# Kernel optimization log

Hardware: AMD Instinct MI355X
Metric: run time of the kernel (lower is better)

Reference implementation:

```python
import jax, jax.numpy as jnp
import numpy as np

LAST_Q = 64      # queries used for dynamic pattern estimation (MInference default)
V_TOPK = 1024    # number of vertical (column) indices kept
S_TOPK = 2048    # number of slash (diagonal) offsets kept
FORCE_V = 30     # first columns always kept
FORCE_S = 100    # most-recent diagonals always kept


def setup_inputs() -> dict:
    key = jax.random.key(0)
    kq, kk, kv = jax.random.split(key, 3)
    B, H, S, D = 1, 8, 4096, 128
    q = jax.random.normal(kq, (B, H, S, D), dtype=jnp.float32)
    k = jax.random.normal(kk, (B, H, S, D), dtype=jnp.float32)
    v = jax.random.normal(kv, (B, H, S, D), dtype=jnp.float32)
    return {"q": q, "k": k, "v": v}


def _vertical_slash_attention(q, k, v):
    B, H, S, D = q.shape
    scale = 1.0 / np.sqrt(D).astype(np.float32)

    # ---- pattern estimation on the last LAST_Q queries ----
    qk = jnp.einsum('bhqd,bhkd->bhqk', q[:, :, -LAST_Q:], k) * scale  # [B,H,LQ,S]
    qpos = S - LAST_Q + jnp.arange(LAST_Q)                            # query positions
    causal_last = qpos[:, None] >= jnp.arange(S)[None, :]             # [LQ,S]
    qk = jnp.where(causal_last, qk, jnp.finfo(qk.dtype).min)
    qk = jax.nn.softmax(qk, axis=-1)

    # vertical (column) scores
    vertical = qk.sum(axis=2)                                         # [B,H,S]
    vertical = vertical.at[..., :FORCE_V].set(jnp.inf)
    v_idx = jax.lax.top_k(vertical, V_TOPK)[1]                        # column ids [B,H,V_TOPK]

    # slash (diagonal) scores, indexed by distance o = i - j in [0, S)
    dist = qpos[:, None] - jnp.arange(S)[None, :]                     # [LQ,S]
    dist_c = jnp.clip(dist, 0, S - 1)
    slash = jnp.zeros((B, H, S), qk.dtype).at[:, :, dist_c].add(
        jnp.where(dist >= 0, qk, 0.0))                                # [B,H,S]
    slash = slash.at[..., :FORCE_S].set(jnp.inf)
    s_off = jax.lax.top_k(slash, S_TOPK)[1]                           # diagonal offsets [B,H,S_TOPK]

    # ---- build vertical-slash sparsity mask ----
    ar = jnp.arange(S)
    v_mask = (v_idx[..., :, None] == ar).any(axis=-2)                 # [B,H,S] column allowed
    s_mask = (s_off[..., :, None] == ar).any(axis=-2)                 # [B,H,S] offset allowed

    dmat = ar[:, None] - ar[None, :]                                  # [S,S] query-key distance
    causal = dmat >= 0
    allowed = causal & (v_mask[:, :, None, :] | s_mask[:, :, jnp.clip(dmat, 0, S - 1)])

    # ---- sparse (mask-equivalent) attention ----
    scores = jnp.einsum('bhqd,bhkd->bhqk', q, k) * scale              # [B,H,S,S]
    scores = jnp.where(allowed, scores, jnp.finfo(scores.dtype).min)
    probs = jax.nn.softmax(scores, axis=-1)
    return jnp.einsum('bhqk,bhkd->bhqd', probs, v)


def reference(q, k, v):
    return _vertical_slash_attention(q, k, v)
```

## Files before the change

kernel.cpp:

```cpp
#include <hip/hip_runtime.h>
#include <hip/hip_bf16.h>
#include <math.h>

#define S_LEN 4096
#define DHEAD 128
#define NHEAD 8
#define LASTQ 64
#define V_TOPK 1024
#define S_TOPK 2048
#define FORCE_V 30
#define FORCE_S 100

#define SCALE 0.08838834764831845f
#define NEGBIG -3.0e38f

typedef __attribute__((ext_vector_type(8))) short short8;
typedef __attribute__((ext_vector_type(4))) float floatx4;
typedef unsigned long long u64;

__device__ __forceinline__ unsigned short f2bf(float f) {
    unsigned u = __float_as_uint(f);
    unsigned r = (u + 0x7fffu + ((u >> 16) & 1u)) >> 16;
    return (unsigned short)r;
}

__global__ __launch_bounds__(256) void cvt_bf16(const float* __restrict__ src,
                                                unsigned short* __restrict__ dst, int n4) {
    int i = blockIdx.x * 256 + threadIdx.x;
    if (i < n4) {
        float4 v = ((const float4*)src)[i];
        ushort4 o;
        o.x = f2bf(v.x); o.y = f2bf(v.y); o.z = f2bf(v.z); o.w = f2bf(v.w);
        ((ushort4*)dst)[i] = o;
    }
}

__global__ __launch_bounds__(256) void transpose_v(const float* __restrict__ v,
                                                   unsigned short* __restrict__ vt) {
    int bx = blockIdx.x;
    int h  = bx >> 7;
    int rem = bx & 127;
    int d0 = (rem >> 6) * 64;
    int k0 = (rem & 63) * 64;
    __shared__ __align__(16) unsigned short T[64][72];
    int t = threadIdx.x;
#pragma unroll
    for (int it = 0; it < 4; ++it) {
        int idx = t + it * 256;
        int r = idx >> 4, c4 = idx & 15;
        float4 val = *(const float4*)(v + ((size_t)(h * S_LEN) + k0 + r) * DHEAD + d0 + c4 * 4);
        T[c4 * 4 + 0][r] = f2bf(val.x);
        T[c4 * 4 + 1][r] = f2bf(val.y);
        T[c4 * 4 + 2][r] = f2bf(val.z);
        T[c4 * 4 + 3][r] = f2bf(val.w);
    }
    __syncthreads();
#pragma unroll
    for (int it = 0; it < 2; ++it) {
        int idx = t + it * 256;
        int r = idx >> 3, c8 = idx & 7;
        *(uint4*)(vt + ((size_t)h * DHEAD + d0 + r) * S_LEN + k0 + c8 * 8) = *(uint4*)&T[r][c8 * 8];
    }
}

__global__ __launch_bounds__(256) void score_qk(const float* __restrict__ q,
                                                const float* __restrict__ k,
                                                float* __restrict__ scores) {
    int h  = blockIdx.x >> 6;
    int kt = blockIdx.x & 63;
    int t  = threadIdx.x;
    int jl = t >> 2, part = t & 3;
    int j  = kt * 64 + jl;

    __shared__ float4 Qs[64 * 32];
    const float4* qbase = (const float4*)(q + ((size_t)h * S_LEN + (S_LEN - LASTQ)) * DHEAD);
    for (int idx = t; idx < 64 * 32; idx += 256) Qs[idx] = qbase[idx];
    __syncthreads();

    float4 kr[8];
    const float4* kp = (const float4*)(k + ((size_t)h * S_LEN + j) * DHEAD) + part * 8;
#pragma unroll
    for (int c = 0; c < 8; ++c) kr[c] = kp[c];

    float* sp = scores + (size_t)h * LASTQ * S_LEN + j;
#pragma unroll 4
    for (int qi = 0; qi < LASTQ; ++qi) {
        const float4* qp4 = Qs + qi * 32 + part * 8;
        float dot = 0.f;
#pragma unroll
        for (int c = 0; c < 8; ++c) {
            float4 a = qp4[c], b = kr[c];
            dot += a.x * b.x + a.y * b.y + a.z * b.z + a.w * b.w;
        }
        dot += __shfl_xor(dot, 1, 64);
        dot += __shfl_xor(dot, 2, 64);
        if (part == 0) {
            int qpos = S_LEN - LASTQ + qi;
            sp[(size_t)qi * S_LEN] = (j <= qpos) ? dot * SCALE : NEGBIG;
        }
    }
}

__global__ __launch_bounds__(256) void row_stats(const float* __restrict__ scores,
                                                 float* __restrict__ m_out,
                                                 float* __restrict__ inv_out) {
    int row  = blockIdx.x * 4 + (threadIdx.x >> 6);
    int lane = threadIdx.x & 63;
    const float4* rp = (const float4*)(scores + (size_t)row * S_LEN);
    float mx = NEGBIG;
    for (int i = lane; i < S_LEN / 4; i += 64) {
        float4 s4 = rp[i];
        mx = fmaxf(mx, fmaxf(fmaxf(s4.x, s4.y), fmaxf(s4.z, s4.w)));
    }
#pragma unroll
    for (int d = 32; d >= 1; d >>= 1) mx = fmaxf(mx, __shfl_xor(mx, d, 64));
    float su = 0.f;
    for (int i = lane; i < S_LEN / 4; i += 64) {
        float4 s4 = rp[i];
        su += __expf(s4.x - mx) + __expf(s4.y - mx) + __expf(s4.z - mx) + __expf(s4.w - mx);
    }
#pragma unroll
    for (int d = 32; d >= 1; d >>= 1) su += __shfl_xor(su, d, 64);
    if (lane == 0) { m_out[row] = mx; inv_out[row] = 1.0f / su; }
}

__global__ __launch_bounds__(256) void vs_accum(const float* __restrict__ scores,
                                                const float* __restrict__ m_all,
                                                const float* __restrict__ inv_all,
                                                float* __restrict__ vertical,
                                                float* __restrict__ slash) {
    int h     = blockIdx.x >> 3;
    int chunk = blockIdx.x & 7;
    int t = threadIdx.x;
    __shared__ float sm[LASTQ], sv[LASTQ];
    if (t < LASTQ) { sm[t] = m_all[h * LASTQ + t]; sv[t] = inv_all[h * LASTQ + t]; }
    __syncthreads();

    const float* S0 = scores + (size_t)h * LASTQ * S_LEN;
#pragma unroll
    for (int rep = 0; rep < 2; ++rep) {
        int j = chunk * 512 + rep * 256 + t;
        float vacc = 0.f, sacc = 0.f;
        for (int r = 0; r < LASTQ; ++r) {
            vacc += __expf(S0[(size_t)r * S_LEN + j] - sm[r]) * sv[r];
            int idx = (S_LEN - LASTQ) + r - j;
            if (idx >= 0)
                sacc += __expf(S0[(size_t)r * S_LEN + idx] - sm[r]) * sv[r];
        }
        vertical[h * S_LEN + j] = vacc;
        slash[h * S_LEN + j]    = sacc;
    }
}

__global__ __launch_bounds__(256) void topk_mask(const float* __restrict__ vertical,
                                                 const float* __restrict__ slash,
                                                 unsigned* __restrict__ col_mask,
                                                 unsigned* __restrict__ diag_mask) {
    int h   = blockIdx.x >> 1;
    int sel = blockIdx.x & 1;
    const float* src = sel ? (slash + h * S_LEN) : (vertical + h * S_LEN);
    unsigned* dst    = sel ? (diag_mask + h * (S_LEN / 32)) : (col_mask + h * (S_LEN / 32));
    int kwant  = sel ? S_TOPK : V_TOPK;
    int forced = sel ? FORCE_S : FORCE_V;
    int t = threadIdx.x;

    __shared__ unsigned keys[S_LEN];
    __shared__ int hist[256];
    __shared__ int sh_digit, sh_want;

    for (int j = t; j < S_LEN; j += 256) {
        float f = (j < forced) ? __builtin_inff() : src[j];
        unsigned u = __float_as_uint(f);
        u = (u & 0x80000000u) ? ~u : (u | 0x80000000u);
        keys[j] = u;
    }
    __syncthreads();

    unsigned prefix = 0;
    int want = kwant;
    for (int shift = 24; shift >= 0; shift -= 8) {
        hist[t] = 0;
        __syncthreads();
        for (int j = t; j < S_LEN; j += 256) {
            unsigned key = keys[j];
            bool match = (shift == 24) || (((key ^ prefix) >> (shift + 8)) == 0);
            if (match) atomicAdd(&hist[(key >> shift) & 255u], 1);
        }
        __syncthreads();
        if (t == 0) {
            int cum = 0, d = 255;
            for (; d >= 0; --d) {
                cum += hist[d];
                if (cum >= want) break;
            }
            sh_digit = d;
            sh_want  = want - (cum - hist[d]);
        }
        __syncthreads();
        prefix |= ((unsigned)sh_digit) << shift;
        want = sh_want;
        __syncthreads();
    }
    for (int w = t; w < S_LEN / 32; w += 256) {
        unsigned bits = 0;
        for (int b = 0; b < 32; ++b)
            if (keys[w * 32 + b] >= prefix) bits |= (1u << b);
        dst[w] = bits;
    }
}

#define KS_STRIDE 136
#define VT_STRIDE 72
#define PS_STRIDE 72

__global__ __launch_bounds__(256, 2) void sparse_attn_mfma(
        const unsigned short* __restrict__ qbf,
        const unsigned short* __restrict__ kbf,
        const unsigned short* __restrict__ vtbf,
        const unsigned* __restrict__ col_mask,
        const unsigned* __restrict__ diag_mask,
        float* __restrict__ pO, float* __restrict__ pm, float* __restrict__ pl) {
    int b = blockIdx.x;
    int h = b & 7;
    int j = b >> 3;
    int qt, c0g, c1g, cidx;
    if (j < 64) {
        qt = 63 - (j >> 1);
        int half = j & 1;
        int mid = (qt + 2) >> 1;
        cidx = half;
        c0g = half ? mid : 0;
        c1g = half ? (qt + 1) : mid;
    } else {
        qt = 95 - j;
        cidx = 0;
        c0g = 0;
        c1g = qt + 1;
    }
    int i0 = qt * 64;
    int t    = threadIdx.x;
    int wave = t >> 6;
    int lane = t & 63;
    int ln16 = lane & 15;
    int quad = lane >> 4;

    __shared__ __align__(16) unsigned short Ks[64 * KS_STRIDE];
    __shared__ __align__(16) unsigned short Vt[128 * VT_STRIDE];
    __shared__ __align__(16) unsigned short Ps[4 * 16 * PS_STRIDE];
    __shared__ u64 allowed[64];
    __shared__ unsigned dmLDS[130];

    if (t < 130) dmLDS[t] = (t < 128) ? diag_mask[h * 128 + t] : 0u;

    int qrow = i0 + wave * 16 + ln16;
    const unsigned short* qp = qbf + ((size_t)h * S_LEN + qrow) * DHEAD;
    short8 qf[4];
#pragma unroll
    for (int ds = 0; ds < 4; ++ds)
        qf[ds] = *(const short8*)(qp + ds * 32 + quad * 8);

    floatx4 o4[8];
#pragma unroll
    for (int n = 0; n < 8; ++n) o4[n] = (floatx4){0.f, 0.f, 0.f, 0.f};
    float m_run[4] = {NEGBIG, NEGBIG, NEGBIG, NEGBIG};
    float l_run[4] = {0.f, 0.f, 0.f, 0.f};

    unsigned short* psw = Ps + wave * 16 * PS_STRIDE;

    for (int jt = c0g; jt < c1g; ++jt) {
        int j0 = jt * 64;
        __syncthreads();

#pragma unroll
        for (int it = 0; it < 4; ++it) {
            int idx = t + it * 256;
            int r = idx >> 4, c8 = idx & 15;
            *(uint4*)&Ks[r * KS_STRIDE + c8 * 8] =
                *(const uint4*)(kbf + ((size_t)(h * S_LEN) + j0 + r) * DHEAD + c8 * 8);
        }
#pragma unroll
        for (int it = 0; it < 4; ++it) {
            int idx = t + it * 256;
            int r = idx >> 3, c8 = idx & 7;
            *(uint4*)&Vt[r * VT_STRIDE + c8 * 8] =
                *(const uint4*)(vtbf + ((size_t)h * DHEAD + r) * S_LEN + j0 + c8 * 8);
        }
        if (t < 64) {
            int i = i0 + t;
            int off0 = i - j0;
            u64 causal = (off0 >= 63) ? ~0ull : ((1ull << (off0 + 1)) - 1ull);
            u64 cwv = ((u64)col_mask[h * 128 + (j0 >> 5) + 1] << 32) |
                      (u64)col_mask[h * 128 + (j0 >> 5)];
            int sb = off0 - 63;
            u64 V;
            if (sb >= 0) {
                int w = sb >> 5, sh = sb & 31;
                u64 lo = ((u64)dmLDS[w + 1] << 32) | (u64)dmLDS[w];
                u64 hi = (u64)dmLDS[w + 2];
                V = (lo >> sh) | (sh ? (hi << (64 - sh)) : 0ull);
            } else {
                u64 w0 = ((u64)dmLDS[1] << 32) | (u64)dmLDS[0];
                V = w0 << (-sb);
            }
            allowed[t] = (cwv | __brevll(V)) & causal;
        }
        __syncthreads();

        floatx4 s_acc[4];
#pragma unroll
        for (int c = 0; c < 4; ++c) {
            s_acc[c] = (floatx4){0.f, 0.f, 0.f, 0.f};
            const unsigned short* kbase = Ks + (c * 16 + ln16) * KS_STRIDE + quad * 8;
#pragma unroll
            for (int ds = 0; ds < 4; ++ds) {
                short8 kf = *(const short8*)(kbase + ds * 32);
                s_acc[c] = __builtin_amdgcn_mfma_f32_16x16x32_bf16(qf[ds], kf, s_acc[c], 0, 0, 0);
            }
        }

        u64 Arow[4];
#pragma unroll
        for (int r = 0; r < 4; ++r)
            Arow[r] = allowed[wave * 16 + quad * 4 + r];
        float sc[4][4];
#pragma unroll
        for (int c = 0; c < 4; ++c)
#pragma unroll
            for (int r = 0; r < 4; ++r) {
                bool ok = (Arow[r] >> (c * 16 + ln16)) & 1ull;
                sc[c][r] = ok ? s_acc[c][r] * SCALE : -__builtin_inff();
            }

        float mnew[4], alpha[4];
#pragma unroll
        for (int r = 0; r < 4; ++r) {
            float mx = fmaxf(fmaxf(sc[0][r], sc[1][r]), fmaxf(sc[2][r], sc[3][r]));
#pragma unroll
            for (int d = 8; d >= 1; d >>= 1) mx = fmaxf(mx, __shfl_xor(mx, d, 64));
            mnew[r] = fmaxf(m_run[r], mx);
            alpha[r] = __expf(m_run[r] - mnew[r]);
            m_run[r] = mnew[r];
        }
        float pv[4][4];
#pragma unroll
        for (int r = 0; r < 4; ++r) {
            float su = 0.f;
#pragma unroll
            for (int c = 0; c < 4; ++c) {
                float p = __expf(sc[c][r] - mnew[r]);
                pv[c][r] = p;
                su += p;
            }
#pragma unroll
            for (int d = 8; d >= 1; d >>= 1) su += __shfl_xor(su, d, 64);
            l_run[r] = l_run[r] * alpha[r] + su;
        }
#pragma unroll
        for (int n = 0; n < 8; ++n)
#pragma unroll
            for (int r = 0; r < 4; ++r) o4[n][r] *= alpha[r];

#pragma unroll
        for (int c = 0; c < 4; ++c)
#pragma unroll
            for (int r = 0; r < 4; ++r)
                psw[(quad * 4 + r) * PS_STRIDE + c * 16 + ln16] = f2bf(pv[c][r]);
        asm volatile("" ::: "memory");
        short8 pf0 = *(const short8*)&psw[ln16 * PS_STRIDE + quad * 8];
        short8 pf1 = *(const short8*)&psw[ln16 * PS_STRIDE + 32 + quad * 8];

#pragma unroll
        for (int n = 0; n < 8; ++n) {
            const unsigned short* vbase = Vt + (n * 16 + ln16) * VT_STRIDE + quad * 8;
            short8 vf0 = *(const short8*)(vbase);
            short8 vf1 = *(const short8*)(vbase + 32);
            o4[n] = __builtin_amdgcn_mfma_f32_16x16x32_bf16(pf0, vf0, o4[n], 0, 0, 0);
            o4[n] = __builtin_amdgcn_mfma_f32_16x16x32_bf16(pf1, vf1, o4[n], 0, 0, 0);
        }
    }

    int pi = (h * 64 + qt) * 2 + cidx;
    float* pOp = pO + (size_t)pi * (64 * DHEAD);
#pragma unroll
    for (int r = 0; r < 4; ++r) {
        int row = wave * 16 + quad * 4 + r;
        if (ln16 == 0) { pm[pi * 64 + row] = m_run[r]; pl[pi * 64 + row] = l_run[r]; }
#pragma unroll
        for (int n = 0; n < 8; ++n)
            pOp[row * DHEAD + n * 16 + ln16] = o4[n][r];
    }
}

__global__ __launch_bounds__(256) void merge_out(const float* __restrict__ pO,
                                                 const float* __restrict__ pm,
                                                 const float* __restrict__ pl,
                                                 float* __restrict__ out) {
    int b = blockIdx.x;
    int qt = b & 63;
    int t = threadIdx.x;
    int row = t >> 2, cg = t & 3;
    int pi0 = b * 2;
    bool two = (qt >= 32);

    float m0 = pm[pi0 * 64 + row], l0 = pl[pi0 * 64 + row];
    float w0 = 1.f, w1 = 0.f, denom = l0;
    if (two) {
        float m1 = pm[(pi0 + 1) * 64 + row], l1 = pl[(pi0 + 1) * 64 + row];
        float ms = fmaxf(m0, m1);
        w0 = __expf(m0 - ms);
        w1 = __expf(m1 - ms);
        denom = w0 * l0 + w1 * l1;
    }
    float invl = 1.0f / denom;

    const float4* O0 = (const float4*)(pO + (size_t)pi0 * (64 * DHEAD) + row * DHEAD + cg * 32);
    const float4* O1 = (const float4*)((const float*)O0 + 64 * DHEAD);
    float4* op = (float4*)(out + ((size_t)b * 64 + row) * DHEAD + cg * 32);
#pragma unroll
    for (int i = 0; i < 8; ++i) {
        float4 a = O0[i];
        float4 c;
        if (two) {
            float4 bb = O1[i];
            c.x = (w0 * a.x + w1 * bb.x) * invl;
            c.y = (w0 * a.y + w1 * bb.y) * invl;
            c.z = (w0 * a.z + w1 * bb.z) * invl;
            c.w = (w0 * a.w + w1 * bb.w) * invl;
        } else {
            c.x = a.x * invl; c.y = a.y * invl; c.z = a.z * invl; c.w = a.w * invl;
        }
        op[i] = c;
    }
}

extern "C" void kernel_launch(void* const* d_in, const int* in_sizes, int n_in,
                              void* d_out, int out_size, void* d_ws, size_t ws_size,
                              hipStream_t stream) {
    const float* q = (const float*)d_in[0];
    const float* k = (const float*)d_in[1];
    const float* v = (const float*)d_in[2];
    float* out = (float*)d_out;

    float* vertical = (float*)d_ws;
    float* slash    = vertical + NHEAD * S_LEN;
    unsigned* col_m  = (unsigned*)(slash + NHEAD * S_LEN);
    unsigned* diag_m = col_m + NHEAD * (S_LEN / 32);
    float* m_all   = (float*)(diag_m + NHEAD * (S_LEN / 32));
    float* inv_all = m_all + NHEAD * LASTQ;
    unsigned short* qbf  = (unsigned short*)(inv_all + NHEAD * LASTQ);
    unsigned short* kbf  = qbf + (size_t)NHEAD * S_LEN * DHEAD;
    unsigned short* vtbf = kbf + (size_t)NHEAD * S_LEN * DHEAD;
    float* big = (float*)(vtbf + (size_t)NHEAD * S_LEN * DHEAD);
    float* scores = big;
    float* pO = big;
    float* pm = big + (size_t)1024 * 64 * DHEAD;
    float* pl = pm + 1024 * 64;

    int n4 = NHEAD * S_LEN * DHEAD / 4;
    cvt_bf16<<<(n4 + 255) / 256, 256, 0, stream>>>(q, qbf, n4);
    cvt_bf16<<<(n4 + 255) / 256, 256, 0, stream>>>(k, kbf, n4);
    transpose_v<<<NHEAD * 2 * (S_LEN / 64), 256, 0, stream>>>(v, vtbf);

    score_qk<<<NHEAD * 64, 256, 0, stream>>>(q, k, scores);
    row_stats<<<NHEAD * LASTQ / 4, 256, 0, stream>>>(scores, m_all, inv_all);
    vs_accum<<<NHEAD * 8, 256, 0, stream>>>(scores, m_all, inv_all, vertical, slash);
    topk_mask<<<NHEAD * 2, 256, 0, stream>>>(vertical, slash, col_m, diag_m);

    sparse_attn_mfma<<<NHEAD * 96, 256, 0, stream>>>(qbf, kbf, vtbf, col_m, diag_m, pO, pm, pl);
    merge_out<<<NHEAD * 64, 256, 0, stream>>>(pO, pm, pl, out);
}
```

Baseline: 362.2 us.

## Restructure sparse attention into 128-row query tiles with balanced split-K job table

The attention kernel now handles 128 query rows per block, with two 16-row sub-tiles per wave that share each K/V tile load. A static job table splits the causal key range into roughly equal chunks so blocks get balanced work. The Q bf16 conversion and scale are folded into the attention kernel, and the K convert and V transpose are merged into one prep launch. The vertical/slash accumulation is fused into the top-k kernel using 1024 threads, and partial outputs are stored as bf16 to cut merge traffic. In exchange, register pressure rises, and rounding the partial outputs to bf16 adds some precision loss.

```diff
diff --git a/kernel.cpp b/kernel.cpp
--- a/kernel.cpp
+++ b/kernel.cpp
@@ -14,6 +14,8 @@
 #define SCALE 0.08838834764831845f
 #define NEGBIG -3.0e38f
 
+#define NJOBS 111
+
 typedef __attribute__((ext_vector_type(8))) short short8;
 typedef __attribute__((ext_vector_type(4))) float floatx4;
 typedef unsigned long long u64;
@@ -23,43 +25,77 @@
     unsigned r = (u + 0x7fffu + ((u >> 16) & 1u)) >> 16;
     return (unsigned short)r;
 }
-
-__global__ __launch_bounds__(256) void cvt_bf16(const float* __restrict__ src,
-                                                unsigned short* __restrict__ dst, int n4) {
-    int i = blockIdx.x * 256 + threadIdx.x;
-    if (i < n4) {
-        float4 v = ((const float4*)src)[i];
-        ushort4 o;
-        o.x = f2bf(v.x); o.y = f2bf(v.y); o.z = f2bf(v.z); o.w = f2bf(v.w);
-        ((ushort4*)dst)[i] = o;
-    }
-}
-
-__global__ __launch_bounds__(256) void transpose_v(const float* __restrict__ v,
-                                                   unsigned short* __restrict__ vt) {
-    int bx = blockIdx.x;
-    int h  = bx >> 7;
-    int rem = bx & 127;
-    int d0 = (rem >> 6) * 64;
-    int k0 = (rem & 63) * 64;
-    __shared__ __align__(16) unsigned short T[64][72];
-    int t = threadIdx.x;
-#pragma unroll
-    for (int it = 0; it < 4; ++it) {
-        int idx = t + it * 256;
-        int r = idx >> 4, c4 = idx & 15;
-        float4 val = *(const float4*)(v + ((size_t)(h * S_LEN) + k0 + r) * DHEAD + d0 + c4 * 4);
-        T[c4 * 4 + 0][r] = f2bf(val.x);
-        T[c4 * 4 + 1][r] = f2bf(val.y);
-        T[c4 * 4 + 2][r] = f2bf(val.z);
-        T[c4 * 4 + 3][r] = f2bf(val.w);
-    }
-    __syncthreads();
-#pragma unroll
-    for (int it = 0; it < 2; ++it) {
-        int idx = t + it * 256;
-        int r = idx >> 3, c8 = idx & 7;
-        *(uint4*)(vt + ((size_t)h * DHEAD + d0 + r) * S_LEN + k0 + c8 * 8) = *(uint4*)&T[r][c8 * 8];
+__device__ __forceinline__ float bf2f(unsigned short s) {
+    unsigned u = ((unsigned)s) << 16;
+    return __uint_as_float(u);
+}
+
+__device__ const short jobQ[NJOBS] = {
+    0,1,2,3,4, 5,5, 6,6, 7,7, 8,8, 9,9, 10,10,
+    11,11,11, 12,12,12, 13,13,13, 14,14,14, 15,15,15,
+    16,16,16,16, 17,17,17,17, 18,18,18,18, 19,19,19,19, 20,20,20,20, 21,21,21,21,
+    22,22,22,22,22, 23,23,23,23,23, 24,24,24,24,24, 25,25,25,25,25, 26,26,26,26,26,
+    27,27,27,27,27,27, 28,28,28,28,28,28, 29,29,29,29,29,29, 30,30,30,30,30,30,
+    31,31,31,31,31,31};
+__device__ const short jobK0[NJOBS] = {
+    0,0,0,0,0, 0,6, 0,7, 0,8, 0,9, 0,10, 0,11,
+    0,8,16, 0,9,18, 0,10,19, 0,10,20, 0,11,22,
+    0,9,18,26, 0,9,18,27, 0,10,20,29, 0,10,20,30, 0,11,22,32, 0,11,22,33,
+    0,10,19,28,37, 0,10,20,30,39, 0,10,20,30,40, 0,11,22,32,42, 0,11,22,33,44,
+    0,10,20,29,38,47, 0,10,20,30,40,49, 0,10,20,30,40,50, 0,11,22,32,42,52,
+    0,11,22,33,44,54};
+__device__ const short jobK1[NJOBS] = {
+    2,4,6,8,10, 6,12, 7,14, 8,16, 9,18, 10,20, 11,22,
+    8,16,24, 9,18,26, 10,19,28, 10,20,30, 11,22,32,
+    9,18,26,34, 9,18,27,36, 10,20,29,38, 10,20,30,40, 11,22,32,42, 11,22,33,44,
+    10,19,28,37,46, 10,20,30,39,48, 10,20,30,40,50, 11,22,32,42,52, 11,22,33,44,54,
+    10,20,29,38,47,56, 10,20,30,40,49,58, 10,20,30,40,50,60, 11,22,32,42,52,62,
+    11,22,33,44,54,64};
+__device__ const short pBase[32] = {0,1,2,3,4,5,7,9,11,13,15,17,20,23,26,29,
+                                    32,36,40,44,48,52,56,61,66,71,76,81,87,93,99,105};
+__device__ const short pCnt[32]  = {1,1,1,1,1,2,2,2,2,2,2,3,3,3,3,3,
+                                    4,4,4,4,4,4,5,5,5,5,5,6,6,6,6,6};
+
+__global__ __launch_bounds__(256) void prep(const float* __restrict__ k,
+                                            const float* __restrict__ v,
+                                            unsigned short* __restrict__ kbf,
+                                            unsigned short* __restrict__ vtbf) {
+    int b = blockIdx.x, t = threadIdx.x;
+    if (b < 512) {
+        const float4* src = (const float4*)k;
+        int base = b * 2048;
+#pragma unroll
+        for (int i = 0; i < 8; ++i) {
+            int idx = base + i * 256 + t;
+            float4 val = src[idx];
+            ushort4 o;
+            o.x = f2bf(val.x); o.y = f2bf(val.y); o.z = f2bf(val.z); o.w = f2bf(val.w);
+            ((ushort4*)kbf)[idx] = o;
+        }
+    } else {
+        int bx = b - 512;
+        int h  = bx >> 7;
+        int rem = bx & 127;
+        int d0 = (rem >> 6) * 64;
+        int k0 = (rem & 63) * 64;
+        __shared__ __align__(16) unsigned short T[64][72];
+#pragma unroll
+        for (int it = 0; it < 4; ++it) {
+            int idx = t + it * 256;
+            int r = idx >> 4, c4 = idx & 15;
+            float4 val = *(const float4*)(v + ((size_t)(h * S_LEN) + k0 + r) * DHEAD + d0 + c4 * 4);
+            T[c4 * 4 + 0][r] = f2bf(val.x);
+            T[c4 * 4 + 1][r] = f2bf(val.y);
+            T[c4 * 4 + 2][r] = f2bf(val.z);
+            T[c4 * 4 + 3][r] = f2bf(val.w);
+        }
+        __syncthreads();
+#pragma unroll
+        for (int it = 0; it < 2; ++it) {
+            int idx = t + it * 256;
+            int r = idx >> 3, c8 = idx & 7;
+            *(uint4*)(vtbf + ((size_t)h * DHEAD + d0 + r) * S_LEN + k0 + c8 * 8) = *(uint4*)&T[r][c8 * 8];
+        }
     }
 }
 
@@ -124,52 +160,42 @@
     if (lane == 0) { m_out[row] = mx; inv_out[row] = 1.0f / su; }
 }
 
-__global__ __launch_bounds__(256) void vs_accum(const float* __restrict__ scores,
-                                                const float* __restrict__ m_all,
-                                                const float* __restrict__ inv_all,
-                                                float* __restrict__ vertical,
-                                                float* __restrict__ slash) {
-    int h     = blockIdx.x >> 3;
-    int chunk = blockIdx.x & 7;
-    int t = threadIdx.x;
-    __shared__ float sm[LASTQ], sv[LASTQ];
-    if (t < LASTQ) { sm[t] = m_all[h * LASTQ + t]; sv[t] = inv_all[h * LASTQ + t]; }
-    __syncthreads();
-
-    const float* S0 = scores + (size_t)h * LASTQ * S_LEN;
-#pragma unroll
-    for (int rep = 0; rep < 2; ++rep) {
-        int j = chunk * 512 + rep * 256 + t;
-        float vacc = 0.f, sacc = 0.f;
-        for (int r = 0; r < LASTQ; ++r) {
-            vacc += __expf(S0[(size_t)r * S_LEN + j] - sm[r]) * sv[r];
-            int idx = (S_LEN - LASTQ) + r - j;
-            if (idx >= 0)
-                sacc += __expf(S0[(size_t)r * S_LEN + idx] - sm[r]) * sv[r];
-        }
-        vertical[h * S_LEN + j] = vacc;
-        slash[h * S_LEN + j]    = sacc;
-    }
-}
-
-__global__ __launch_bounds__(256) void topk_mask(const float* __restrict__ vertical,
-                                                 const float* __restrict__ slash,
-                                                 unsigned* __restrict__ col_mask,
-                                                 unsigned* __restrict__ diag_mask) {
+__global__ __launch_bounds__(1024) void pattern_finish(const float* __restrict__ scores,
+                                                       const float* __restrict__ m_all,
+                                                       const float* __restrict__ inv_all,
+                                                       unsigned* __restrict__ col_mask,
+                                                       unsigned* __restrict__ diag_mask) {
     int h   = blockIdx.x >> 1;
     int sel = blockIdx.x & 1;
-    const float* src = sel ? (slash + h * S_LEN) : (vertical + h * S_LEN);
-    unsigned* dst    = sel ? (diag_mask + h * (S_LEN / 32)) : (col_mask + h * (S_LEN / 32));
+    int t = threadIdx.x;
     int kwant  = sel ? S_TOPK : V_TOPK;
     int forced = sel ? FORCE_S : FORCE_V;
-    int t = threadIdx.x;
-
+    unsigned* dst = sel ? (diag_mask + h * 128) : (col_mask + h * 128);
+
+    __shared__ float sm[LASTQ], sv[LASTQ];
     __shared__ unsigned keys[S_LEN];
     __shared__ int hist[256];
     __shared__ int sh_digit, sh_want;
 
-    for (int j = t; j < S_LEN; j += 256) {
-        float f = (j < forced) ? __builtin_inff() : src[j];
+    if (t < LASTQ) { sm[t] = m_all[h * LASTQ + t]; sv[t] = inv_all[h * LASTQ + t]; }
+    __syncthreads();
+
+    const float* S0 = scores + (size_t)h * LASTQ * S_LEN;
+#pragma unroll
+    for (int rep = 0; rep < 4; ++rep) {
+        int j = rep * 1024 + t;
+        float acc = 0.f;
+        if (sel == 0) {
+            for (int r = 0; r < LASTQ; ++r)
+                acc += __expf(S0[(size_t)r * S_LEN + j] - sm[r]) * sv[r];
+        } else {
+            for (int r = 0; r < LASTQ; ++r) {
+                int idx = (S_LEN - LASTQ) + r - j;
+                if (idx >= 0)
+                    acc += __expf(S0[(size_t)r * S_LEN + idx] - sm[r]) * sv[r];
+            }
+        }
+        float f = (j < forced) ? __builtin_inff() : acc;
         unsigned u = __float_as_uint(f);
         u = (u & 0x80000000u) ? ~u : (u | 0x80000000u);
         keys[j] = u;
@@ -179,9 +205,9 @@
     unsigned prefix = 0;
     int want = kwant;
     for (int shift = 24; shift >= 0; shift -= 8) {
-        hist[t] = 0;
-        __syncthreads();
-        for (int j = t; j < S_LEN; j += 256) {
+        if (t < 256) hist[t] = 0;
+        __syncthreads();
+        for (int j = t; j < S_LEN; j += 1024) {
             unsigned key = keys[j];
             bool match = (shift == 24) || (((key ^ prefix) >> (shift + 8)) == 0);
             if (match) atomicAdd(&hist[(key >> shift) & 255u], 1);
@@ -201,11 +227,11 @@
         want = sh_want;
         __syncthreads();
     }
-    for (int w = t; w < S_LEN / 32; w += 256) {
+    if (t < 128) {
         unsigned bits = 0;
         for (int b = 0; b < 32; ++b)
-            if (keys[w * 32 + b] >= prefix) bits |= (1u << b);
-        dst[w] = bits;
+            if (keys[t * 32 + b] >= prefix) bits |= (1u << b);
+        dst[t] = bits;
     }
 }
 
@@ -214,30 +240,19 @@
 #define PS_STRIDE 72
 
 __global__ __launch_bounds__(256, 2) void sparse_attn_mfma(
-        const unsigned short* __restrict__ qbf,
+        const float* __restrict__ q,
         const unsigned short* __restrict__ kbf,
         const unsigned short* __restrict__ vtbf,
         const unsigned* __restrict__ col_mask,
         const unsigned* __restrict__ diag_mask,
-        float* __restrict__ pO, float* __restrict__ pm, float* __restrict__ pl) {
+        unsigned short* __restrict__ pO, float* __restrict__ pm, float* __restrict__ pl) {
     int b = blockIdx.x;
     int h = b & 7;
-    int j = b >> 3;
-    int qt, c0g, c1g, cidx;
-    if (j < 64) {
-        qt = 63 - (j >> 1);
-        int half = j & 1;
-        int mid = (qt + 2) >> 1;
-        cidx = half;
-        c0g = half ? mid : 0;
-        c1g = half ? (qt + 1) : mid;
-    } else {
-        qt = 95 - j;
-        cidx = 0;
-        c0g = 0;
-        c1g = qt + 1;
-    }
-    int i0 = qt * 64;
+    int job = b >> 3;
+    int Q  = jobQ[job];
+    int k0 = jobK0[job];
+    int k1 = jobK1[job];
+    int i0 = Q * 128;
     int t    = threadIdx.x;
     int wave = t >> 6;
     int lane = t & 63;
@@ -246,28 +261,44 @@
 
     __shared__ __align__(16) unsigned short Ks[64 * KS_STRIDE];
     __shared__ __align__(16) unsigned short Vt[128 * VT_STRIDE];
-    __shared__ __align__(16) unsigned short Ps[4 * 16 * PS_STRIDE];
-    __shared__ u64 allowed[64];
+    __shared__ __align__(16) unsigned short Ps[8 * 16 * PS_STRIDE];
+    __shared__ u64 allowed[128];
     __shared__ unsigned dmLDS[130];
 
     if (t < 130) dmLDS[t] = (t < 128) ? diag_mask[h * 128 + t] : 0u;
 
-    int qrow = i0 + wave * 16 + ln16;
-    const unsigned short* qp = qbf + ((size_t)h * S_LEN + qrow) * DHEAD;
-    short8 qf[4];
-#pragma unroll
-    for (int ds = 0; ds < 4; ++ds)
-        qf[ds] = *(const short8*)(qp + ds * 32 + quad * 8);
-
-    floatx4 o4[8];
-#pragma unroll
-    for (int n = 0; n < 8; ++n) o4[n] = (floatx4){0.f, 0.f, 0.f, 0.f};
-    float m_run[4] = {NEGBIG, NEGBIG, NEGBIG, NEGBIG};
-    float l_run[4] = {0.f, 0.f, 0.f, 0.f};
-
-    unsigned short* psw = Ps + wave * 16 * PS_STRIDE;
-
-    for (int jt = c0g; jt < c1g; ++jt) {
+    short8 qf[2][4];
+#pragma unroll
+    for (int s = 0; s < 2; ++s) {
+        int qrow = i0 + wave * 32 + s * 16 + ln16;
+        const float* qp = q + ((size_t)h * S_LEN + qrow) * DHEAD;
+#pragma unroll
+        for (int ds = 0; ds < 4; ++ds) {
+            int base = ds * 32 + quad * 8;
+            float4 a = *(const float4*)(qp + base);
+            float4 c = *(const float4*)(qp + base + 4);
+            union { unsigned short u[8]; short8 v; } tmp;
+            tmp.u[0] = f2bf(a.x * SCALE); tmp.u[1] = f2bf(a.y * SCALE);
+            tmp.u[2] = f2bf(a.z * SCALE); tmp.u[3] = f2bf(a.w * SCALE);
+            tmp.u[4] = f2bf(c.x * SCALE); tmp.u[5] = f2bf(c.y * SCALE);
+            tmp.u[6] = f2bf(c.z * SCALE); tmp.u[7] = f2bf(c.w * SCALE);
+            qf[s][ds] = tmp.v;
+        }
+    }
+
+    floatx4 o4[2][8];
+#pragma unroll
+    for (int s = 0; s < 2; ++s)
+#pragma unroll
+        for (int n = 0; n < 8; ++n) o4[s][n] = (floatx4){0.f, 0.f, 0.f, 0.f};
+    float m_run[2][4] = {{NEGBIG, NEGBIG, NEGBIG, NEGBIG}, {NEGBIG, NEGBIG, NEGBIG, NEGBIG}};
+    float l_run[2][4] = {{0.f, 0.f, 0.f, 0.f}, {0.f, 0.f, 0.f, 0.f}};
+
+    unsigned short* psw[2];
+    psw[0] = Ps + (wave * 2 + 0) * 16 * PS_STRIDE;
+    psw[1] = Ps + (wave * 2 + 1) * 16 * PS_STRIDE;
+
+    for (int jt = k0; jt < k1; ++jt) {
         int j0 = jt * 64;
         __syncthreads();
 
@@ -285,151 +316,179 @@
             *(uint4*)&Vt[r * VT_STRIDE + c8 * 8] =
                 *(const uint4*)(vtbf + ((size_t)h * DHEAD + r) * S_LEN + j0 + c8 * 8);
         }
-        if (t < 64) {
+        if (t < 128) {
             int i = i0 + t;
             int off0 = i - j0;
-            u64 causal = (off0 >= 63) ? ~0ull : ((1ull << (off0 + 1)) - 1ull);
-            u64 cwv = ((u64)col_mask[h * 128 + (j0 >> 5) + 1] << 32) |
-                      (u64)col_mask[h * 128 + (j0 >> 5)];
-            int sb = off0 - 63;
-            u64 V;
-            if (sb >= 0) {
-                int w = sb >> 5, sh = sb & 31;
-                u64 lo = ((u64)dmLDS[w + 1] << 32) | (u64)dmLDS[w];
-                u64 hi = (u64)dmLDS[w + 2];
-                V = (lo >> sh) | (sh ? (hi << (64 - sh)) : 0ull);
-            } else {
-                u64 w0 = ((u64)dmLDS[1] << 32) | (u64)dmLDS[0];
-                V = w0 << (-sb);
-            }
-            allowed[t] = (cwv | __brevll(V)) & causal;
-        }
-        __syncthreads();
-
-        floatx4 s_acc[4];
+            u64 a = 0;
+            if (off0 >= 0) {
+                u64 causal = (off0 >= 63) ? ~0ull : ((1ull << (off0 + 1)) - 1ull);
+                u64 cwv = ((u64)col_mask[h * 128 + (j0 >> 5) + 1] << 32) |
+                          (u64)col_mask[h * 128 + (j0 >> 5)];
+                int sb = off0 - 63;
+                u64 V;
+                if (sb >= 0) {
+                    int w = sb >> 5, sh = sb & 31;
+                    u64 lo = ((u64)dmLDS[w + 1] << 32) | (u64)dmLDS[w];
+                    u64 hi = (u64)dmLDS[w + 2];
+                    V = (lo >> sh) | (sh ? (hi << (64 - sh)) : 0ull);
+                } else {
+                    u64 w0 = ((u64)dmLDS[1] << 32) | (u64)dmLDS[0];
+                    V = w0 << (-sb);
+                }
+                a = (cwv | __brevll(V)) & causal;
+            }
+            allowed[t] = a;
+        }
+        __syncthreads();
+
+        floatx4 sa[2][4];
+#pragma unroll
+        for (int s = 0; s < 2; ++s)
+#pragma unroll
+            for (int c = 0; c < 4; ++c) sa[s][c] = (floatx4){0.f, 0.f, 0.f, 0.f};
 #pragma unroll
         for (int c = 0; c < 4; ++c) {
-            s_acc[c] = (floatx4){0.f, 0.f, 0.f, 0.f};
             const unsigned short* kbase = Ks + (c * 16 + ln16) * KS_STRIDE + quad * 8;
 #pragma unroll
             for (int ds = 0; ds < 4; ++ds) {
                 short8 kf = *(const short8*)(kbase + ds * 32);
-                s_acc[c] = __builtin_amdgcn_mfma_f32_16x16x32_bf16(qf[ds], kf, s_acc[c], 0, 0, 0);
-            }
-        }
-
-        u64 Arow[4];
-#pragma unroll
-        for (int r = 0; r < 4; ++r)
-            Arow[r] = allowed[wave * 16 + quad * 4 + r];
-        float sc[4][4];
-#pragma unroll
-        for (int c = 0; c < 4; ++c)
+                sa[0][c] = __builtin_amdgcn_mfma_f32_16x16x32_bf16(qf[0][ds], kf, sa[0][c], 0, 0, 0);
+                sa[1][c] = __builtin_amdgcn_mfma_f32_16x16x32_bf16(qf[1][ds], kf, sa[1][c], 0, 0, 0);
+            }
+        }
+
+#pragma unroll
+        for (int s = 0; s < 2; ++s) {
+            u64 Arow[4];
+#pragma unroll
+            for (int r = 0; r < 4; ++r)
+                Arow[r] = allowed[wave * 32 + s * 16 + quad * 4 + r];
+            float sc[4][4];
+#pragma unroll
+            for (int c = 0; c < 4; ++c)
+#pragma unroll
+                for (int r = 0; r < 4; ++r) {
+                    bool ok = (Arow[r] >> (c * 16 + ln16)) & 1ull;
+                    sc[c][r] = ok ? sa[s][c][r] : -__builtin_inff();
+                }
+            float mnew[4], alpha[4];
 #pragma unroll
             for (int r = 0; r < 4; ++r) {
-                bool ok = (Arow[r] >> (c * 16 + ln16)) & 1ull;
-                sc[c][r] = ok ? s_acc[c][r] * SCALE : -__builtin_inff();
-            }
-
-        float mnew[4], alpha[4];
-#pragma unroll
-        for (int r = 0; r < 4; ++r) {
-            float mx = fmaxf(fmaxf(sc[0][r], sc[1][r]), fmaxf(sc[2][r], sc[3][r]));
-#pragma unroll
-            for (int d = 8; d >= 1; d >>= 1) mx = fmaxf(mx, __shfl_xor(mx, d, 64));
-            mnew[r] = fmaxf(m_run[r], mx);
-            alpha[r] = __expf(m_run[r] - mnew[r]);
-            m_run[r] = mnew[r];
-        }
-        float pv[4][4];
-#pragma unroll
-        for (int r = 0; r < 4; ++r) {
-            float su = 0.f;
-#pragma unroll
-            for (int c = 0; c < 4; ++c) {
-                float p = __expf(sc[c][r] - mnew[r]);
-                pv[c][r] = p;
-                su += p;
-            }
-#pragma unroll
-            for (int d = 8; d >= 1; d >>= 1) su += __shfl_xor(su, d, 64);
-            l_run[r] = l_run[r] * alpha[r] + su;
-        }
-#pragma unroll
-        for (int n = 0; n < 8; ++n)
-#pragma unroll
-            for (int r = 0; r < 4; ++r) o4[n][r] *= alpha[r];
-
-#pragma unroll
-        for (int c = 0; c < 4; ++c)
-#pragma unroll
-            for (int r = 0; r < 4; ++r)
-                psw[(quad * 4 + r) * PS_STRIDE + c * 16 + ln16] = f2bf(pv[c][r]);
+                float mx = fmaxf(fmaxf(sc[0][r], sc[1][r]), fmaxf(sc[2][r], sc[3][r]));
+#pragma unroll
+                for (int d = 8; d >= 1; d >>= 1) mx = fmaxf(mx, __shfl_xor(mx, d, 64));
+                mnew[r] = fmaxf(m_run[s][r], mx);
+                alpha[r] = __expf(m_run[s][r] - mnew[r]);
+                m_run[s][r] = mnew[r];
+            }
+#pragma unroll
+            for (int r = 0; r < 4; ++r) {
+                float su = 0.f;
+                float pvr[4];
+#pragma unroll
+                for (int c = 0; c < 4; ++c) {
+                    float p = __expf(sc[c][r] - mnew[r]);
+                    pvr[c] = p;
+                    su += p;
+                }
+#pragma unroll
+                for (int c = 0; c < 4; ++c)
+                    psw[s][(quad * 4 + r) * PS_STRIDE + c * 16 + ln16] = f2bf(pvr[c]);
+#pragma unroll
+                for (int d = 8; d >= 1; d >>= 1) su += __shfl_xor(su, d, 64);
+                l_run[s][r] = l_run[s][r] * alpha[r] + su;
+            }
+#pragma unroll
+            for (int n = 0; n < 8; ++n)
+#pragma unroll
+                for (int r = 0; r < 4; ++r) o4[s][n][r] *= alpha[r];
+        }
         asm volatile("" ::: "memory");
-        short8 pf0 = *(const short8*)&psw[ln16 * PS_STRIDE + quad * 8];
-        short8 pf1 = *(const short8*)&psw[ln16 * PS_STRIDE + 32 + quad * 8];
+
+        short8 pf[2][2];
+#pragma unroll
+        for (int s = 0; s < 2; ++s) {
+            pf[s][0] = *(const short8*)&psw[s][ln16 * PS_STRIDE + quad * 8];
+            pf[s][1] = *(const short8*)&psw[s][ln16 * PS_STRIDE + 32 + quad * 8];
+        }
 
 #pragma unroll
         for (int n = 0; n < 8; ++n) {
             const unsigned short* vbase = Vt + (n * 16 + ln16) * VT_STRIDE + quad * 8;
             short8 vf0 = *(const short8*)(vbase);
             short8 vf1 = *(const short8*)(vbase + 32);
-            o4[n] = __builtin_amdgcn_mfma_f32_16x16x32_bf16(pf0, vf0, o4[n], 0, 0, 0);
-            o4[n] = __builtin_amdgcn_mfma_f32_16x16x32_bf16(pf1, vf1, o4[n], 0, 0, 0);
-        }
-    }
-
-    int pi = (h * 64 + qt) * 2 + cidx;
-    float* pOp = pO + (size_t)pi * (64 * DHEAD);
-#pragma unroll
-    for (int r = 0; r < 4; ++r) {
-        int row = wave * 16 + quad * 4 + r;
-        if (ln16 == 0) { pm[pi * 64 + row] = m_run[r]; pl[pi * 64 + row] = l_run[r]; }
-#pragma unroll
-        for (int n = 0; n < 8; ++n)
-            pOp[row * DHEAD + n * 16 + ln16] = o4[n][r];
-    }
-}
-
-__global__ __launch_bounds__(256) void merge_out(const float* __restrict__ pO,
+            o4[0][n] = __builtin_amdgcn_mfma_f32_16x16x32_bf16(pf[0][0], vf0, o4[0][n], 0, 0, 0);
+            o4[0][n] = __builtin_amdgcn_mfma_f32_16x16x32_bf16(pf[0][1], vf1, o4[0][n], 0, 0, 0);
+            o4[1][n] = __builtin_amdgcn_mfma_f32_16x16x32_bf16(pf[1][0], vf0, o4[1][n], 0, 0, 0);
+            o4[1][n] = __builtin_amdgcn_mfma_f32_16x16x32_bf16(pf[1][1], vf1, o4[1][n], 0, 0, 0);
+        }
+    }
+
+    int pidx = h * NJOBS + job;
+    unsigned short* pOp = pO + (size_t)pidx * (128 * DHEAD);
+#pragma unroll
+    for (int s = 0; s < 2; ++s)
+#pragma unroll
+        for (int r = 0; r < 4; ++r) {
+            int row = wave * 32 + s * 16 + quad * 4 + r;
+            if (ln16 == 0) {
+                pm[pidx * 128 + row] = m_run[s][r];
+                pl[pidx * 128 + row] = l_run[s][r];
+            }
+#pragma unroll
+            for (int n = 0; n < 8; ++n)
+                pOp[row * DHEAD + n * 16 + ln16] = f2bf(o4[s][n][r]);
+        }
+}
+
+__global__ __launch_bounds__(256) void merge_out(const unsigned short* __restrict__ pO,
                                                  const float* __restrict__ pm,
                                                  const float* __restrict__ pl,
                                                  float* __restrict__ out) {
     int b = blockIdx.x;
-    int qt = b & 63;
+    int h = b >> 5, Q = b & 31;
     int t = threadIdx.x;
-    int row = t >> 2, cg = t & 3;
-    int pi0 = b * 2;
-    bool two = (qt >= 32);
-
-    float m0 = pm[pi0 * 64 + row], l0 = pl[pi0 * 64 + row];
-    float w0 = 1.f, w1 = 0.f, denom = l0;
-    if (two) {
-        float m1 = pm[(pi0 + 1) * 64 + row], l1 = pl[(pi0 + 1) * 64 + row];
-        float ms = fmaxf(m0, m1);
-        w0 = __expf(m0 - ms);
-        w1 = __expf(m1 - ms);
-        denom = w0 * l0 + w1 * l1;
+    int row = t >> 1, half = t & 1;
+    int p0 = h * NJOBS + pBase[Q];
+    int cnt = pCnt[Q];
+
+    float mp[6], lp[6];
+    float ms = NEGBIG;
+    for (int p = 0; p < cnt; ++p) {
+        mp[p] = pm[(p0 + p) * 128 + row];
+        lp[p] = pl[(p0 + p) * 128 + row];
+        ms = fmaxf(ms, mp[p]);
+    }
+    float denom = 0.f, w[6];
+    for (int p = 0; p < cnt; ++p) {
+        w[p] = __expf(mp[p] - ms);
+        denom += w[p] * lp[p];
     }
     float invl = 1.0f / denom;
 
-    const float4* O0 = (const float4*)(pO + (size_t)pi0 * (64 * DHEAD) + row * DHEAD + cg * 32);
-    const float4* O1 = (const float4*)((const float*)O0 + 64 * DHEAD);
-    float4* op = (float4*)(out + ((size_t)b * 64 + row) * DHEAD + cg * 32);
-#pragma unroll
-    for (int i = 0; i < 8; ++i) {
-        float4 a = O0[i];
+    float acc[64];
+#pragma unroll
+    for (int i = 0; i < 64; ++i) acc[i] = 0.f;
+    for (int p = 0; p < cnt; ++p) {
+        const unsigned short* Op = pO + (size_t)(p0 + p) * (128 * DHEAD) + row * DHEAD + half * 64;
+        float wp = w[p];
+#pragma unroll
+        for (int g = 0; g < 8; ++g) {
+            ushort4 u0 = ((const ushort4*)Op)[g * 2];
+            ushort4 u1 = ((const ushort4*)Op)[g * 2 + 1];
+            acc[g * 8 + 0] += wp * bf2f(u0.x); acc[g * 8 + 1] += wp * bf2f(u0.y);
+            acc[g * 8 + 2] += wp * bf2f(u0.z); acc[g * 8 + 3] += wp * bf2f(u0.w);
+            acc[g * 8 + 4] += wp * bf2f(u1.x); acc[g * 8 + 5] += wp * bf2f(u1.y);
+            acc[g * 8 + 6] += wp * bf2f(u1.z); acc[g * 8 + 7] += wp * bf2f(u1.w);
+        }
+    }
+    float* op = out + ((size_t)h * S_LEN + Q * 128 + row) * DHEAD + half * 64;
+#pragma unroll
+    for (int g = 0; g < 16; ++g) {
         float4 c;
-        if (two) {
-            float4 bb = O1[i];
-            c.x = (w0 * a.x + w1 * bb.x) * invl;
-            c.y = (w0 * a.y + w1 * bb.y) * invl;
-            c.z = (w0 * a.z + w1 * bb.z) * invl;
-            c.w = (w0 * a.w + w1 * bb.w) * invl;
-        } else {
-            c.x = a.x * invl; c.y = a.y * invl; c.z = a.z * invl; c.w = a.w * invl;
-        }
-        op[i] = c;
+        c.x = acc[g * 4 + 0] * invl; c.y = acc[g * 4 + 1] * invl;
+        c.z = acc[g * 4 + 2] * invl; c.w = acc[g * 4 + 3] * invl;
+        ((float4*)op)[g] = c;
     }
 }
 
@@ -441,31 +500,21 @@
     const float* v = (const float*)d_in[2];
     float* out = (float*)d_out;
 
-    float* vertical = (float*)d_ws;
-    float* slash    = vertical + NHEAD * S_LEN;
-    unsigned* col_m  = (unsigned*)(slash + NHEAD * S_LEN);
-    unsigned* diag_m = col_m + NHEAD * (S_LEN / 32);
-    float* m_all   = (float*)(diag_m + NHEAD * (S_LEN / 32));
-    float* inv_all = m_all + NHEAD * LASTQ;
-    unsigned short* qbf  = (unsigned short*)(inv_all + NHEAD * LASTQ);
-    unsigned short* kbf  = qbf + (size_t)NHEAD * S_LEN * DHEAD;
+    unsigned* col_m  = (unsigned*)d_ws;
+    unsigned* diag_m = col_m + 1024;
+    float* m_all   = (float*)(diag_m + 1024);
+    float* inv_all = m_all + 512;
+    unsigned short* kbf  = (unsigned short*)(inv_all + 512);
     unsigned short* vtbf = kbf + (size_t)NHEAD * S_LEN * DHEAD;
-    float* big = (float*)(vtbf + (size_t)NHEAD * S_LEN * DHEAD);
-    float* scores = big;
-    float* pO = big;
-    float* pm = big + (size_t)1024 * 64 * DHEAD;
-    float* pl = pm + 1024 * 64;
-
-    int n4 = NHEAD * S_LEN * DHEAD / 4;
-    cvt_bf16<<<(n4 + 255) / 256, 256, 0, stream>>>(q, qbf, n4);
-    cvt_bf16<<<(n4 + 255) / 256, 256, 0, stream>>>(k, kbf, n4);
-    transpose_v<<<NHEAD * 2 * (S_LEN / 64), 256, 0, stream>>>(v, vtbf);
-
+    float* scores = (float*)(vtbf + (size_t)NHEAD * S_LEN * DHEAD);
+    unsigned short* pO = (unsigned short*)(scores + (size_t)NHEAD * LASTQ * S_LEN);
+    float* pm = (float*)(pO + (size_t)8 * NJOBS * 128 * DHEAD);
+    float* pl = pm + 8 * NJOBS * 128;
+
+    prep<<<1536, 256, 0, stream>>>(k, v, kbf, vtbf);
     score_qk<<<NHEAD * 64, 256, 0, stream>>>(q, k, scores);
     row_stats<<<NHEAD * LASTQ / 4, 256, 0, stream>>>(scores, m_all, inv_all);
-    vs_accum<<<NHEAD * 8, 256, 0, stream>>>(scores, m_all, inv_all, vertical, slash);
-    topk_mask<<<NHEAD * 2, 256, 0, stream>>>(vertical, slash, col_m, diag_m);
-
-    sparse_attn_mfma<<<NHEAD * 96, 256, 0, stream>>>(qbf, kbf, vtbf, col_m, diag_m, pO, pm, pl);
-    merge_out<<<NHEAD * 64, 256, 0, stream>>>(pO, pm, pl, out);
-}
+    pattern_finish<<<NHEAD * 2, 1024, 0, stream>>>(scores, m_all, inv_all, col_m, diag_m);
+    sparse_attn_mfma<<<NHEAD * NJOBS, 256, 0, stream>>>(q, kbf, vtbf, col_m, diag_m, pO, pm, pl);
+    merge_out<<<NHEAD * 32, 256, 0, stream>>>(pO, pm, pl, out);
+}
```

New measurement: 300.9 us. 16.9% less time.
